# Kernel optimization log

Hardware: AMD Instinct MI355X
Metric: run time of the kernel (lower is better)

The kernel has to match this reference:

```python
import jax, jax.numpy as jnp
import numpy as np

# Levi-Civita tensor for the 1e x 1e -> 1e CG path (component normalization: eps/sqrt(2))
_e = np.zeros((3, 3, 3), dtype=np.float32)
_e[0, 1, 2] = _e[1, 2, 0] = _e[2, 0, 1] = 1.0
_e[0, 2, 1] = _e[2, 1, 0] = _e[1, 0, 2] = -1.0
EPS = jnp.asarray(_e)

B = 400000
M1S, M1V = 16, 8    # site irreps: 16x0e + 8x1e
MES, MEV = 4, 4     # edge irreps: 4x0e + 4x1e


def _split(x, mul_s, mul_v):
    # flat e3nn layout: scalars first, then vectors (xyz blocks)
    return x[:, :mul_s], x[:, mul_s:].reshape(x.shape[0], mul_v, 3)


def _fctp(x0, x1, y0, y1, W00, W11_0, W01, W10, W11_1):
    """FullyConnectedTensorProduct over irreps {0e,1e} x {0e,1e} -> {0e,1e}.
    x0:[B,u], x1:[B,u,3], y0:[B,v], y1:[B,v,3]."""
    fan0 = W00.shape[0] * W00.shape[1] + W11_0.shape[0] * W11_0.shape[1]
    out0 = (jnp.einsum('bu,bv,uvw->bw', x0, y0, W00)
            + jnp.einsum('bui,bvi,uvw->bw', x1, y1, W11_0) / np.sqrt(3.0)) / np.sqrt(fan0)
    fan1 = (W01.shape[0] * W01.shape[1] + W10.shape[0] * W10.shape[1]
            + W11_1.shape[0] * W11_1.shape[1])
    cross = jnp.einsum('bui,bvj,ijk->buvk', x1, y1, EPS)  # [B,u,v,3]
    out1 = (jnp.einsum('bu,bvi,uvw->bwi', x0, y1, W01)
            + jnp.einsum('bui,bv,uvw->bwi', x1, y0, W10)
            + jnp.einsum('buvk,uvw->bwk', cross, W11_1) / np.sqrt(2.0)) / np.sqrt(fan1)
    return out0, out1


def _forward(site1, site2, edge,
             W1_00, W1_11_0, W1_01, W1_10, W1_11_1,
             W2_00, W2_11_0, W2_01, W2_10, W2_11_1,
             W3_00, W3_11):
    x0, x1 = _split(site1, M1S, M1V)
    y0, y1 = _split(site2, M1S, M1V)
    # node-node tensor product -> 32x0e + 16x1e
    t0, t1 = _fctp(x0, x1, y0, y1, W1_00, W1_11_0, W1_01, W1_10, W1_11_1)
    e0, e1 = _split(edge, MES, MEV)
    # node-node-edge tensor product -> 64x0e + 32x1e
    u0, u1 = _fctp(t0, t1, e0, e1, W2_00, W2_11_0, W2_01, W2_10, W2_11_1)
    # Gate: 32 scalars (silu) | 32 gates (sigmoid) gating 32x1e
    s = jax.nn.silu(u0[:, :32])
    g = jax.nn.sigmoid(u0[:, 32:])
    v = u1 * g[:, :, None]
    # TensorSquare -> 1x0e (component normalization)
    fan = W3_00.shape[0] * W3_00.shape[1] + W3_11.shape[0] * W3_11.shape[1]
    out = (jnp.einsum('bu,bv,uvw->bw', s, s, W3_00)
           + jnp.einsum('bui,bvi,uvw->bw', v, v, W3_11) / np.sqrt(3.0)) / np.sqrt(fan)
    return out


def setup_inputs() -> dict:
    key = jax.random.key(0)
    ks = jax.random.split(key, 16)
    f32 = jnp.float32
    return {
        'site1': jax.random.normal(ks[0], (B, M1S + 3 * M1V), f32),
        'site2': jax.random.normal(ks[1], (B, M1S + 3 * M1V), f32),
        'edge': jax.random.normal(ks[2], (B, MES + 3 * MEV), f32),
        'W1_00': jax.random.normal(ks[3], (16, 16, 32), f32),
        'W1_11_0': jax.random.normal(ks[4], (8, 8, 32), f32),
        'W1_01': jax.random.normal(ks[5], (16, 8, 16), f32),
        'W1_10': jax.random.normal(ks[6], (8, 16, 16), f32),
        'W1_11_1': jax.random.normal(ks[7], (8, 8, 16), f32),
        'W2_00': jax.random.normal(ks[8], (32, 4, 64), f32),
        'W2_11_0': jax.random.normal(ks[9], (16, 4, 64), f32),
        'W2_01': jax.random.normal(ks[10], (32, 4, 32), f32),
        'W2_10': jax.random.normal(ks[11], (16, 4, 32), f32),
        'W2_11_1': jax.random.normal(ks[12], (16, 4, 32), f32),
        'W3_00': jax.random.normal(ks[13], (32, 32, 1), f32),
        'W3_11': jax.random.normal(ks[14], (32, 32, 1), f32),
    }


def reference(site1, site2, edge,
              W1_00, W1_11_0, W1_01, W1_10, W1_11_1,
              W2_00, W2_11_0, W2_01, W2_10, W2_11_1,
              W3_00, W3_11):
    return _forward(site1, site2, edge,
                    W1_00, W1_11_0, W1_01, W1_10, W1_11_1,
                    W2_00, W2_11_0, W2_01, W2_10, W2_11_1,
                    W3_00, W3_11)
```

## Files before the change

### kernel.cpp

```cpp
#include <hip/hip_runtime.h>


#define TPB 128

__device__ __forceinline__ float sigf(float x) {
    return 1.0f / (1.0f + __expf(-x));
}

__global__ __launch_bounds__(TPB, 2)
void intersite_fused(const float* __restrict__ site1,
                     const float* __restrict__ site2,
                     const float* __restrict__ edge,
                     const float* __restrict__ W1_00,
                     const float* __restrict__ W1_11_0,
                     const float* __restrict__ W1_01,
                     const float* __restrict__ W1_10,
                     const float* __restrict__ W1_11_1,
                     const float* __restrict__ W2_00,
                     const float* __restrict__ W2_11_0,
                     const float* __restrict__ W2_01,
                     const float* __restrict__ W2_10,
                     const float* __restrict__ W2_11_1,
                     const float* __restrict__ W3_00,
                     const float* __restrict__ W3_11,
                     float* __restrict__ out, int B)
{
    __shared__ float lds[80 * TPB];
    const int t = threadIdx.x;
    const int b = blockIdx.x * TPB + t;
    if (b >= B) return;

#define LDSF(f) lds[(f) * TPB + t]

    const float inv_s3   = 0.57735026918962576f;
    const float inv_s2   = 0.70710678118654752f;
    const float inv_s320 = 0.05590169943749474f;
    const float inv_s192 = 0.07216878364870323f;
    const float inv_s256 = 0.0625f;
    const float inv_s2048= 0.02209708691207961f;

    {
        const float4* p1 = (const float4*)(site1 + (size_t)b * 40);
        #pragma unroll
        for (int q = 0; q < 10; ++q) {
            float4 r = p1[q];
            LDSF(q*4+0) = r.x; LDSF(q*4+1) = r.y;
            LDSF(q*4+2) = r.z; LDSF(q*4+3) = r.w;
        }
        const float4* p2 = (const float4*)(site2 + (size_t)b * 40);
        #pragma unroll
        for (int q = 0; q < 10; ++q) {
            float4 r = p2[q];
            LDSF(40+q*4+0) = r.x; LDSF(40+q*4+1) = r.y;
            LDSF(40+q*4+2) = r.z; LDSF(40+q*4+3) = r.w;
        }
    }

    float t0[32];
    #pragma unroll
    for (int k = 0; k < 32; ++k) t0[k] = 0.0f;

    #pragma unroll 1
    for (int u = 0; u < 16; ++u) {
        float xu = LDSF(u);
        const float* wu = W1_00 + u * 512;
        #pragma unroll
        for (int v = 0; v < 16; ++v) {
            float f = xu * LDSF(40 + v);
            #pragma unroll
            for (int k = 0; k < 32; ++k) t0[k] = fmaf(f, wu[v*32+k], t0[k]);
        }
    }
    #pragma unroll 1
    for (int u = 0; u < 8; ++u) {
        float ax = LDSF(16+u*3), ay = LDSF(17+u*3), az = LDSF(18+u*3);
        const float* wu = W1_11_0 + u * 256;
        #pragma unroll
        for (int v = 0; v < 8; ++v) {
            float d = ax * LDSF(56+v*3);
            d = fmaf(ay, LDSF(57+v*3), d);
            d = fmaf(az, LDSF(58+v*3), d);
            d *= inv_s3;
            #pragma unroll
            for (int k = 0; k < 32; ++k) t0[k] = fmaf(d, wu[v*32+k], t0[k]);
        }
    }
    #pragma unroll
    for (int k = 0; k < 32; ++k) t0[k] *= inv_s320;

    float t1[48];
    #pragma unroll
    for (int j = 0; j < 48; ++j) t1[j] = 0.0f;

    #pragma unroll 1
    for (int u = 0; u < 16; ++u) {
        float xu = LDSF(u);
        const float* wu = W1_01 + u * 128;
        #pragma unroll
        for (int v = 0; v < 8; ++v) {
            float f0 = xu * LDSF(56+v*3+0);
            float f1 = xu * LDSF(56+v*3+1);
            float f2 = xu * LDSF(56+v*3+2);
            #pragma unroll
            for (int k = 0; k < 16; ++k) {
                float w = wu[v*16+k];
                t1[k*3+0] = fmaf(f0, w, t1[k*3+0]);
                t1[k*3+1] = fmaf(f1, w, t1[k*3+1]);
                t1[k*3+2] = fmaf(f2, w, t1[k*3+2]);
            }
        }
    }
    #pragma unroll 1
    for (int u = 0; u < 8; ++u) {
        float ax = LDSF(16+u*3), ay = LDSF(17+u*3), az = LDSF(18+u*3);
        const float* wu = W1_10 + u * 256;
        #pragma unroll
        for (int v = 0; v < 16; ++v) {
            float yv = LDSF(40 + v);
            float f0 = ax*yv, f1 = ay*yv, f2 = az*yv;
            #pragma unroll
            for (int k = 0; k < 16; ++k) {
                float w = wu[v*16+k];
                t1[k*3+0] = fmaf(f0, w, t1[k*3+0]);
                t1[k*3+1] = fmaf(f1, w, t1[k*3+1]);
                t1[k*3+2] = fmaf(f2, w, t1[k*3+2]);
            }
        }
    }
    #pragma unroll 1
    for (int u = 0; u < 8; ++u) {
        float ax = LDSF(16+u*3), ay = LDSF(17+u*3), az = LDSF(18+u*3);
        const float* wu = W1_11_1 + u * 128;
        #pragma unroll
        for (int v = 0; v < 8; ++v) {
            float bx = LDSF(56+v*3), by = LDSF(57+v*3), bz = LDSF(58+v*3);
            float cx = (ay*bz - az*by) * inv_s2;
            float cy = (az*bx - ax*bz) * inv_s2;
            float cz = (ax*by - ay*bx) * inv_s2;
            #pragma unroll
            for (int k = 0; k < 16; ++k) {
                float w = wu[v*16+k];
                t1[k*3+0] = fmaf(cx, w, t1[k*3+0]);
                t1[k*3+1] = fmaf(cy, w, t1[k*3+1]);
                t1[k*3+2] = fmaf(cz, w, t1[k*3+2]);
            }
        }
    }
    #pragma unroll
    for (int j = 0; j < 48; ++j) t1[j] *= inv_s320;

    #pragma unroll
    for (int k = 0; k < 32; ++k) LDSF(k) = t0[k];
    #pragma unroll
    for (int j = 0; j < 48; ++j) LDSF(32 + j) = t1[j];

    float e0r[4], e1r[12];
    {
        const float4* pe = (const float4*)(edge + (size_t)b * 16);
        float4 r0 = pe[0], r1 = pe[1], r2 = pe[2], r3 = pe[3];
        e0r[0]=r0.x; e0r[1]=r0.y; e0r[2]=r0.z; e0r[3]=r0.w;
        e1r[0]=r1.x; e1r[1]=r1.y; e1r[2]=r1.z; e1r[3]=r1.w;
        e1r[4]=r2.x; e1r[5]=r2.y; e1r[6]=r2.z; e1r[7]=r2.w;
        e1r[8]=r3.x; e1r[9]=r3.y; e1r[10]=r3.z; e1r[11]=r3.w;
    }

    float acc0 = 0.0f;
    {
        float ua[32];
        #pragma unroll
        for (int k = 0; k < 32; ++k) ua[k] = 0.0f;
        #pragma unroll 2
        for (int u = 0; u < 32; ++u) {
            float tu = LDSF(u);
            const float* wu = W2_00 + u*256;
            #pragma unroll
            for (int v = 0; v < 4; ++v) {
                float f = tu * e0r[v];
                #pragma unroll
                for (int k = 0; k < 32; ++k) ua[k] = fmaf(f, wu[v*64+k], ua[k]);
            }
        }
        #pragma unroll 2
        for (int u = 0; u < 16; ++u) {
            float a0 = LDSF(32+u*3), a1 = LDSF(33+u*3), a2 = LDSF(34+u*3);
            const float* wu = W2_11_0 + u*256;
            #pragma unroll
            for (int v = 0; v < 4; ++v) {
                float d = a0 * e1r[v*3];
                d = fmaf(a1, e1r[v*3+1], d);
                d = fmaf(a2, e1r[v*3+2], d);
                d *= inv_s3;
                #pragma unroll
                for (int k = 0; k < 32; ++k) ua[k] = fmaf(d, wu[v*64+k], ua[k]);
            }
        }
        #pragma unroll
        for (int k = 0; k < 32; ++k) {
            float x = ua[k] * inv_s192;
            ua[k] = x * sigf(x);
        }
        float zs[32];
        #pragma unroll
        for (int k = 0; k < 32; ++k) zs[k] = 0.0f;
        #pragma unroll
        for (int u = 0; u < 32; ++u) {
            const float* w = W3_00 + u*32;
            #pragma unroll
            for (int k = 0; k < 32; ++k) zs[k] = fmaf(ua[u], w[k], zs[k]);
        }
        #pragma unroll
        for (int k = 0; k < 32; ++k) acc0 = fmaf(zs[k], ua[k], acc0);
    }

    float g[32];
    {
        float ub[32];
        #pragma unroll
        for (int k = 0; k < 32; ++k) ub[k] = 0.0f;
        #pragma unroll 2
        for (int u = 0; u < 32; ++u) {
            float tu = LDSF(u);
            const float* wu = W2_00 + u*256 + 32;
            #pragma unroll
            for (int v = 0; v < 4; ++v) {
                float f = tu * e0r[v];
                #pragma unroll
                for (int k = 0; k < 32; ++k) ub[k] = fmaf(f, wu[v*64+k], ub[k]);
            }
        }
        #pragma unroll 2
        for (int u = 0; u < 16; ++u) {
            float a0 = LDSF(32+u*3), a1 = LDSF(33+u*3), a2 = LDSF(34+u*3);
            const float* wu = W2_11_0 + u*256 + 32;
            #pragma unroll
            for (int v = 0; v < 4; ++v) {
                float d = a0 * e1r[v*3];
                d = fmaf(a1, e1r[v*3+1], d);
                d = fmaf(a2, e1r[v*3+2], d);
                d *= inv_s3;
                #pragma unroll
                for (int k = 0; k < 32; ++k) ub[k] = fmaf(d, wu[v*64+k], ub[k]);
            }
        }
        #pragma unroll
        for (int k = 0; k < 32; ++k) g[k] = sigf(ub[k] * inv_s192);
    }

    float acc1 = 0.0f;
    const float* ep = edge + (size_t)b * 16 + 4;
    #pragma unroll 1
    for (int i = 0; i < 3; ++i) {
        int jj = (i == 2) ? 0 : i + 1;
        int kk = (jj == 2) ? 0 : jj + 1;
        float e1i[4], e1j[4], e1k[4];
        #pragma unroll
        for (int v = 0; v < 4; ++v) {
            e1i[v] = ep[v*3 + i];
            e1j[v] = ep[v*3 + jj];
            e1k[v] = ep[v*3 + kk];
        }
        float u1i[32];
        #pragma unroll
        for (int k = 0; k < 32; ++k) u1i[k] = 0.0f;

        #pragma unroll 2
        for (int u = 0; u < 32; ++u) {
            float tu = LDSF(u);
            const float* wu = W2_01 + u*128;
            #pragma unroll
            for (int v = 0; v < 4; ++v) {
                float f = tu * e1i[v];
                #pragma unroll
                for (int k = 0; k < 32; ++k) u1i[k] = fmaf(f, wu[v*32+k], u1i[k]);
            }
        }
        #pragma unroll 2
        for (int u = 0; u < 16; ++u) {
            float ai = LDSF(32 + u*3 + i);
            const float* wu = W2_10 + u*128;
            #pragma unroll
            for (int v = 0; v < 4; ++v) {
                float f = ai * e0r[v];
                #pragma unroll
                for (int k = 0; k < 32; ++k) u1i[k] = fmaf(f, wu[v*32+k], u1i[k]);
            }
        }
        #pragma unroll 2
        for (int u = 0; u < 16; ++u) {
            float aj = LDSF(32 + u*3 + jj);
            float ak = LDSF(32 + u*3 + kk);
            const float* wu = W2_11_1 + u*128;
            #pragma unroll
            for (int v = 0; v < 4; ++v) {
                float c = (aj * e1k[v] - ak * e1j[v]) * inv_s2;
                #pragma unroll
                for (int k = 0; k < 32; ++k) u1i[k] = fmaf(c, wu[v*32+k], u1i[k]);
            }
        }
        #pragma unroll
        for (int k = 0; k < 32; ++k) u1i[k] = u1i[k] * inv_s256 * g[k];
        float zv[32];
        #pragma unroll
        for (int k = 0; k < 32; ++k) zv[k] = 0.0f;
        #pragma unroll
        for (int u = 0; u < 32; ++u) {
            const float* w = W3_11 + u*32;
            #pragma unroll
            for (int k = 0; k < 32; ++k) zv[k] = fmaf(u1i[u], w[k], zv[k]);
        }
        #pragma unroll
        for (int k = 0; k < 32; ++k) acc1 = fmaf(zv[k], u1i[k], acc1);
    }

    out[b] = (acc0 + acc1 * inv_s3) * inv_s2048;
#undef LDSF
}

extern "C" void kernel_launch(void* const* d_in, const int* in_sizes, int n_in,
                              void* d_out, int out_size, void* d_ws, size_t ws_size,
                              hipStream_t stream)
{
    const float* site1   = (const float*)d_in[0];
    const float* site2   = (const float*)d_in[1];
    const float* edge    = (const float*)d_in[2];
    const float* W1_00   = (const float*)d_in[3];
    const float* W1_11_0 = (const float*)d_in[4];
    const float* W1_01   = (const float*)d_in[5];
    const float* W1_10   = (const float*)d_in[6];
    const float* W1_11_1 = (const float*)d_in[7];
    const float* W2_00   = (const float*)d_in[8];
    const float* W2_11_0 = (const float*)d_in[9];
    const float* W2_01   = (const float*)d_in[10];
    const float* W2_10   = (const float*)d_in[11];
    const float* W2_11_1 = (const float*)d_in[12];
    const float* W3_00   = (const float*)d_in[13];
    const float* W3_11   = (const float*)d_in[14];
    float* out = (float*)d_out;

    const int B = in_sizes[0] / 40;
    dim3 grid((B + TPB - 1) / TPB), block(TPB);
    hipLaunchKernelGGL(intersite_fused, grid, block, 0, stream,
                       site1, site2, edge,
                       W1_00, W1_11_0, W1_01, W1_10, W1_11_1,
                       W2_00, W2_11_0, W2_01, W2_10, W2_11_1,
                       W3_00, W3_11, out, B);
}
```

Baseline: 1.292 ms.

## Merge TP loops, precompute edge-independent W2_01 contraction, and split W3 quadratic form

Merges the first tensor product's separate u-loops so each x scalar and vector is read once per u, computing t0 and t1 together. The second stage now accumulates all 64 scalar outputs in one pass instead of two, and precomputes A2 = t0·W2_01 (128 values) once rather than recomputing it for each of the three xyz components. It also fuses the W2_10 and W2_11_1 loops and splits the W3 quadratic form into halves to reduce live registers. The cost is higher register pressure from the 64- and 128-element arrays, which risks spilling or lower occupancy.

```diff
diff --git a/kernel.cpp b/kernel.cpp
--- a/kernel.cpp
+++ b/kernel.cpp
@@ -59,22 +59,39 @@
     float t0[32];
     #pragma unroll
     for (int k = 0; k < 32; ++k) t0[k] = 0.0f;
+    float t1[48];
+    #pragma unroll
+    for (int j = 0; j < 48; ++j) t1[j] = 0.0f;
 
     #pragma unroll 1
     for (int u = 0; u < 16; ++u) {
         float xu = LDSF(u);
-        const float* wu = W1_00 + u * 512;
+        const float* w00 = W1_00 + u * 512;
         #pragma unroll
         for (int v = 0; v < 16; ++v) {
             float f = xu * LDSF(40 + v);
             #pragma unroll
-            for (int k = 0; k < 32; ++k) t0[k] = fmaf(f, wu[v*32+k], t0[k]);
+            for (int k = 0; k < 32; ++k) t0[k] = fmaf(f, w00[v*32+k], t0[k]);
+        }
+        const float* w01 = W1_01 + u * 128;
+        #pragma unroll
+        for (int v = 0; v < 8; ++v) {
+            float f0 = xu * LDSF(56+v*3+0);
+            float f1 = xu * LDSF(56+v*3+1);
+            float f2 = xu * LDSF(56+v*3+2);
+            #pragma unroll
+            for (int k = 0; k < 16; ++k) {
+                float w = w01[v*16+k];
+                t1[k*3+0] = fmaf(f0, w, t1[k*3+0]);
+                t1[k*3+1] = fmaf(f1, w, t1[k*3+1]);
+                t1[k*3+2] = fmaf(f2, w, t1[k*3+2]);
+            }
         }
     }
     #pragma unroll 1
     for (int u = 0; u < 8; ++u) {
         float ax = LDSF(16+u*3), ay = LDSF(17+u*3), az = LDSF(18+u*3);
-        const float* wu = W1_11_0 + u * 256;
+        const float* w110 = W1_11_0 + u * 256;
         #pragma unroll
         for (int v = 0; v < 8; ++v) {
             float d = ax * LDSF(56+v*3);
@@ -82,55 +99,22 @@
             d = fmaf(az, LDSF(58+v*3), d);
             d *= inv_s3;
             #pragma unroll
-            for (int k = 0; k < 32; ++k) t0[k] = fmaf(d, wu[v*32+k], t0[k]);
-        }
-    }
-    #pragma unroll
-    for (int k = 0; k < 32; ++k) t0[k] *= inv_s320;
-
-    float t1[48];
-    #pragma unroll
-    for (int j = 0; j < 48; ++j) t1[j] = 0.0f;
-
-    #pragma unroll 1
-    for (int u = 0; u < 16; ++u) {
-        float xu = LDSF(u);
-        const float* wu = W1_01 + u * 128;
-        #pragma unroll
-        for (int v = 0; v < 8; ++v) {
-            float f0 = xu * LDSF(56+v*3+0);
-            float f1 = xu * LDSF(56+v*3+1);
-            float f2 = xu * LDSF(56+v*3+2);
+            for (int k = 0; k < 32; ++k) t0[k] = fmaf(d, w110[v*32+k], t0[k]);
+        }
+        const float* w10 = W1_10 + u * 256;
+        #pragma unroll
+        for (int v = 0; v < 16; ++v) {
+            float yv = LDSF(40 + v);
+            float f0 = ax*yv, f1 = ay*yv, f2 = az*yv;
             #pragma unroll
             for (int k = 0; k < 16; ++k) {
-                float w = wu[v*16+k];
+                float w = w10[v*16+k];
                 t1[k*3+0] = fmaf(f0, w, t1[k*3+0]);
                 t1[k*3+1] = fmaf(f1, w, t1[k*3+1]);
                 t1[k*3+2] = fmaf(f2, w, t1[k*3+2]);
             }
         }
-    }
-    #pragma unroll 1
-    for (int u = 0; u < 8; ++u) {
-        float ax = LDSF(16+u*3), ay = LDSF(17+u*3), az = LDSF(18+u*3);
-        const float* wu = W1_10 + u * 256;
-        #pragma unroll
-        for (int v = 0; v < 16; ++v) {
-            float yv = LDSF(40 + v);
-            float f0 = ax*yv, f1 = ay*yv, f2 = az*yv;
-            #pragma unroll
-            for (int k = 0; k < 16; ++k) {
-                float w = wu[v*16+k];
-                t1[k*3+0] = fmaf(f0, w, t1[k*3+0]);
-                t1[k*3+1] = fmaf(f1, w, t1[k*3+1]);
-                t1[k*3+2] = fmaf(f2, w, t1[k*3+2]);
-            }
-        }
-    }
-    #pragma unroll 1
-    for (int u = 0; u < 8; ++u) {
-        float ax = LDSF(16+u*3), ay = LDSF(17+u*3), az = LDSF(18+u*3);
-        const float* wu = W1_11_1 + u * 128;
+        const float* w111 = W1_11_1 + u * 128;
         #pragma unroll
         for (int v = 0; v < 8; ++v) {
             float bx = LDSF(56+v*3), by = LDSF(57+v*3), bz = LDSF(58+v*3);
@@ -139,13 +123,15 @@
             float cz = (ax*by - ay*bx) * inv_s2;
             #pragma unroll
             for (int k = 0; k < 16; ++k) {
-                float w = wu[v*16+k];
+                float w = w111[v*16+k];
                 t1[k*3+0] = fmaf(cx, w, t1[k*3+0]);
                 t1[k*3+1] = fmaf(cy, w, t1[k*3+1]);
                 t1[k*3+2] = fmaf(cz, w, t1[k*3+2]);
             }
         }
     }
+    #pragma unroll
+    for (int k = 0; k < 32; ++k) t0[k] *= inv_s320;
     #pragma unroll
     for (int j = 0; j < 48; ++j) t1[j] *= inv_s320;
 
@@ -164,86 +150,68 @@
         e1r[8]=r3.x; e1r[9]=r3.y; e1r[10]=r3.z; e1r[11]=r3.w;
     }
 
+    float u0a[64];
+    #pragma unroll
+    for (int k = 0; k < 64; ++k) u0a[k] = 0.0f;
+    #pragma unroll 2
+    for (int u = 0; u < 32; ++u) {
+        float tu = LDSF(u);
+        const float* wu = W2_00 + u*256;
+        #pragma unroll
+        for (int v = 0; v < 4; ++v) {
+            float f = tu * e0r[v];
+            #pragma unroll
+            for (int k = 0; k < 64; ++k) u0a[k] = fmaf(f, wu[v*64+k], u0a[k]);
+        }
+    }
+    #pragma unroll 2
+    for (int u = 0; u < 16; ++u) {
+        float a0 = LDSF(32+u*3), a1 = LDSF(33+u*3), a2 = LDSF(34+u*3);
+        const float* wu = W2_11_0 + u*256;
+        #pragma unroll
+        for (int v = 0; v < 4; ++v) {
+            float d = a0 * e1r[v*3];
+            d = fmaf(a1, e1r[v*3+1], d);
+            d = fmaf(a2, e1r[v*3+2], d);
+            d *= inv_s3;
+            #pragma unroll
+            for (int k = 0; k < 64; ++k) u0a[k] = fmaf(d, wu[v*64+k], u0a[k]);
+        }
+    }
+
+    float g[32];
+    #pragma unroll
+    for (int k = 0; k < 32; ++k) g[k] = sigf(u0a[32+k] * inv_s192);
+    #pragma unroll
+    for (int k = 0; k < 32; ++k) {
+        float x = u0a[k] * inv_s192;
+        u0a[k] = x * sigf(x);
+    }
     float acc0 = 0.0f;
-    {
-        float ua[32];
-        #pragma unroll
-        for (int k = 0; k < 32; ++k) ua[k] = 0.0f;
-        #pragma unroll 2
+    #pragma unroll
+    for (int h = 0; h < 2; ++h) {
+        float zs[16];
+        #pragma unroll
+        for (int j = 0; j < 16; ++j) zs[j] = 0.0f;
+        #pragma unroll
         for (int u = 0; u < 32; ++u) {
-            float tu = LDSF(u);
-            const float* wu = W2_00 + u*256;
-            #pragma unroll
-            for (int v = 0; v < 4; ++v) {
-                float f = tu * e0r[v];
-                #pragma unroll
-                for (int k = 0; k < 32; ++k) ua[k] = fmaf(f, wu[v*64+k], ua[k]);
-            }
-        }
-        #pragma unroll 2
-        for (int u = 0; u < 16; ++u) {
-            float a0 = LDSF(32+u*3), a1 = LDSF(33+u*3), a2 = LDSF(34+u*3);
-            const float* wu = W2_11_0 + u*256;
-            #pragma unroll
-            for (int v = 0; v < 4; ++v) {
-                float d = a0 * e1r[v*3];
-                d = fmaf(a1, e1r[v*3+1], d);
-                d = fmaf(a2, e1r[v*3+2], d);
-                d *= inv_s3;
-                #pragma unroll
-                for (int k = 0; k < 32; ++k) ua[k] = fmaf(d, wu[v*64+k], ua[k]);
-            }
-        }
-        #pragma unroll
-        for (int k = 0; k < 32; ++k) {
-            float x = ua[k] * inv_s192;
-            ua[k] = x * sigf(x);
-        }
-        float zs[32];
-        #pragma unroll
-        for (int k = 0; k < 32; ++k) zs[k] = 0.0f;
-        #pragma unroll
-        for (int u = 0; u < 32; ++u) {
-            const float* w = W3_00 + u*32;
-            #pragma unroll
-            for (int k = 0; k < 32; ++k) zs[k] = fmaf(ua[u], w[k], zs[k]);
-        }
-        #pragma unroll
-        for (int k = 0; k < 32; ++k) acc0 = fmaf(zs[k], ua[k], acc0);
-    }
-
-    float g[32];
-    {
-        float ub[32];
-        #pragma unroll
-        for (int k = 0; k < 32; ++k) ub[k] = 0.0f;
-        #pragma unroll 2
-        for (int u = 0; u < 32; ++u) {
-            float tu = LDSF(u);
-            const float* wu = W2_00 + u*256 + 32;
-            #pragma unroll
-            for (int v = 0; v < 4; ++v) {
-                float f = tu * e0r[v];
-                #pragma unroll
-                for (int k = 0; k < 32; ++k) ub[k] = fmaf(f, wu[v*64+k], ub[k]);
-            }
-        }
-        #pragma unroll 2
-        for (int u = 0; u < 16; ++u) {
-            float a0 = LDSF(32+u*3), a1 = LDSF(33+u*3), a2 = LDSF(34+u*3);
-            const float* wu = W2_11_0 + u*256 + 32;
-            #pragma unroll
-            for (int v = 0; v < 4; ++v) {
-                float d = a0 * e1r[v*3];
-                d = fmaf(a1, e1r[v*3+1], d);
-                d = fmaf(a2, e1r[v*3+2], d);
-                d *= inv_s3;
-                #pragma unroll
-                for (int k = 0; k < 32; ++k) ub[k] = fmaf(d, wu[v*64+k], ub[k]);
-            }
-        }
-        #pragma unroll
-        for (int k = 0; k < 32; ++k) g[k] = sigf(ub[k] * inv_s192);
+            const float* w = W3_00 + u*32 + h*16;
+            #pragma unroll
+            for (int j = 0; j < 16; ++j) zs[j] = fmaf(u0a[u], w[j], zs[j]);
+        }
+        #pragma unroll
+        for (int j = 0; j < 16; ++j) acc0 = fmaf(zs[j], u0a[h*16+j], acc0);
+    }
+
+    float A2[128];
+    #pragma unroll
+    for (int j = 0; j < 128; ++j) A2[j] = 0.0f;
+    #pragma unroll 4
+    for (int u = 0; u < 32; ++u) {
+        float tu = LDSF(u);
+        const float* w = W2_01 + u*128;
+        #pragma unroll
+        for (int j = 0; j < 128; ++j) A2[j] = fmaf(tu, w[j], A2[j]);
     }
 
     float acc1 = 0.0f;
@@ -252,64 +220,54 @@
     for (int i = 0; i < 3; ++i) {
         int jj = (i == 2) ? 0 : i + 1;
         int kk = (jj == 2) ? 0 : jj + 1;
-        float e1i[4], e1j[4], e1k[4];
+        float e1i[4], e1j[4], e1k4[4];
         #pragma unroll
         for (int v = 0; v < 4; ++v) {
-            e1i[v] = ep[v*3 + i];
-            e1j[v] = ep[v*3 + jj];
-            e1k[v] = ep[v*3 + kk];
+            e1i[v]  = ep[v*3 + i];
+            e1j[v]  = ep[v*3 + jj];
+            e1k4[v] = ep[v*3 + kk];
         }
         float u1i[32];
         #pragma unroll
-        for (int k = 0; k < 32; ++k) u1i[k] = 0.0f;
-
-        #pragma unroll 2
-        for (int u = 0; u < 32; ++u) {
-            float tu = LDSF(u);
-            const float* wu = W2_01 + u*128;
-            #pragma unroll
-            for (int v = 0; v < 4; ++v) {
-                float f = tu * e1i[v];
-                #pragma unroll
-                for (int k = 0; k < 32; ++k) u1i[k] = fmaf(f, wu[v*32+k], u1i[k]);
-            }
-        }
+        for (int k = 0; k < 32; ++k) u1i[k] = A2[k] * e1i[0];
+        #pragma unroll
+        for (int v = 1; v < 4; ++v)
+            #pragma unroll
+            for (int k = 0; k < 32; ++k)
+                u1i[k] = fmaf(A2[v*32+k], e1i[v], u1i[k]);
+
         #pragma unroll 2
         for (int u = 0; u < 16; ++u) {
             float ai = LDSF(32 + u*3 + i);
-            const float* wu = W2_10 + u*128;
+            float aj = LDSF(32 + u*3 + jj);
+            float ak = LDSF(32 + u*3 + kk);
+            const float* wa = W2_10   + u*128;
+            const float* wb = W2_11_1 + u*128;
             #pragma unroll
             for (int v = 0; v < 4; ++v) {
                 float f = ai * e0r[v];
+                float c = (aj * e1k4[v] - ak * e1j[v]) * inv_s2;
                 #pragma unroll
-                for (int k = 0; k < 32; ++k) u1i[k] = fmaf(f, wu[v*32+k], u1i[k]);
-            }
-        }
-        #pragma unroll 2
-        for (int u = 0; u < 16; ++u) {
-            float aj = LDSF(32 + u*3 + jj);
-            float ak = LDSF(32 + u*3 + kk);
-            const float* wu = W2_11_1 + u*128;
-            #pragma unroll
-            for (int v = 0; v < 4; ++v) {
-                float c = (aj * e1k[v] - ak * e1j[v]) * inv_s2;
+                for (int k = 0; k < 32; ++k)
+                    u1i[k] = fmaf(f, wa[v*32+k], fmaf(c, wb[v*32+k], u1i[k]));
+            }
+        }
+        #pragma unroll
+        for (int k = 0; k < 32; ++k) u1i[k] = u1i[k] * inv_s256 * g[k];
+        #pragma unroll
+        for (int h = 0; h < 2; ++h) {
+            float zv[16];
+            #pragma unroll
+            for (int j = 0; j < 16; ++j) zv[j] = 0.0f;
+            #pragma unroll
+            for (int u = 0; u < 32; ++u) {
+                const float* w = W3_11 + u*32 + h*16;
                 #pragma unroll
-                for (int k = 0; k < 32; ++k) u1i[k] = fmaf(c, wu[v*32+k], u1i[k]);
-            }
-        }
-        #pragma unroll
-        for (int k = 0; k < 32; ++k) u1i[k] = u1i[k] * inv_s256 * g[k];
-        float zv[32];
-        #pragma unroll
-        for (int k = 0; k < 32; ++k) zv[k] = 0.0f;
-        #pragma unroll
-        for (int u = 0; u < 32; ++u) {
-            const float* w = W3_11 + u*32;
-            #pragma unroll
-            for (int k = 0; k < 32; ++k) zv[k] = fmaf(u1i[u], w[k], zv[k]);
-        }
-        #pragma unroll
-        for (int k = 0; k < 32; ++k) acc1 = fmaf(zv[k], u1i[k], acc1);
+                for (int j = 0; j < 16; ++j) zv[j] = fmaf(u1i[u], w[j], zv[j]);
+            }
+            #pragma unroll
+            for (int j = 0; j < 16; ++j) acc1 = fmaf(zv[j], u1i[h*16+j], acc1);
+        }
     }
 
     out[b] = (acc0 + acc1 * inv_s3) * inv_s2048;
```

Result: slower. 1.848 ms (+43.0%).

## Store per-thread LDS staging in fp16, keep site2 in registers, raise occupancy

Applied to the files above, without the earlier changes.

The per-thread LDS staging is halved by storing site1 and the intermediate t0/t1 activations as packed half2 instead of float. site2 scalars and vectors now live in registers rather than LDS. Launch bounds go from 2 to 4 blocks per SM to use the freed LDS. Stage 1 is reordered to compute t1 before t0, and the W2_10 and W2_11_1 loops are fused. The aim is higher occupancy and less LDS traffic, at the cost of fp16 rounding of intermediates (accuracy risk) and more register pressure from the added register arrays under the tighter launch bound.

```diff
diff --git a/kernel.cpp b/kernel.cpp
--- a/kernel.cpp
+++ b/kernel.cpp
@@ -1,4 +1,5 @@
 #include <hip/hip_runtime.h>
+#include <hip/hip_fp16.h>
 
 
 #define TPB 128
@@ -7,7 +8,7 @@
     return 1.0f / (1.0f + __expf(-x));
 }
 
-__global__ __launch_bounds__(TPB, 2)
+__global__ __launch_bounds__(TPB, 4)
 void intersite_fused(const float* __restrict__ site1,
                      const float* __restrict__ site2,
                      const float* __restrict__ edge,
@@ -25,12 +26,15 @@
                      const float* __restrict__ W3_11,
                      float* __restrict__ out, int B)
 {
-    __shared__ float lds[80 * TPB];
+    __shared__ float lds[44 * TPB];
     const int t = threadIdx.x;
     const int b = blockIdx.x * TPB + t;
     if (b >= B) return;
 
-#define LDSF(f) lds[(f) * TPB + t]
+    const __half* ph = (const __half*)lds;
+    __half2* ph2 = (__half2*)lds;
+#define RDH(H) __half2float(ph[(((((H) >> 1) * TPB) + t) << 1) | ((H) & 1)])
+#define WRH2(D, a, bb) ph2[(D) * TPB + t] = __floats2half2_rn((a), (bb))
 
     const float inv_s3   = 0.57735026918962576f;
     const float inv_s2   = 0.70710678118654752f;
@@ -44,17 +48,82 @@
         #pragma unroll
         for (int q = 0; q < 10; ++q) {
             float4 r = p1[q];
-            LDSF(q*4+0) = r.x; LDSF(q*4+1) = r.y;
-            LDSF(q*4+2) = r.z; LDSF(q*4+3) = r.w;
-        }
+            WRH2(q*2+0, r.x, r.y);
+            WRH2(q*2+1, r.z, r.w);
+        }
+    }
+    float y0r[16], y1r[24];
+    {
         const float4* p2 = (const float4*)(site2 + (size_t)b * 40);
         #pragma unroll
-        for (int q = 0; q < 10; ++q) {
+        for (int q = 0; q < 4; ++q) {
             float4 r = p2[q];
-            LDSF(40+q*4+0) = r.x; LDSF(40+q*4+1) = r.y;
-            LDSF(40+q*4+2) = r.z; LDSF(40+q*4+3) = r.w;
-        }
-    }
+            y0r[q*4+0]=r.x; y0r[q*4+1]=r.y; y0r[q*4+2]=r.z; y0r[q*4+3]=r.w;
+        }
+        #pragma unroll
+        for (int q = 0; q < 6; ++q) {
+            float4 r = p2[4+q];
+            y1r[q*4+0]=r.x; y1r[q*4+1]=r.y; y1r[q*4+2]=r.z; y1r[q*4+3]=r.w;
+        }
+    }
+
+    float t1[48];
+    #pragma unroll
+    for (int j = 0; j < 48; ++j) t1[j] = 0.0f;
+
+    #pragma unroll 1
+    for (int u = 0; u < 16; ++u) {
+        float xu = RDH(u);
+        const float* w01 = W1_01 + u * 128;
+        #pragma unroll
+        for (int v = 0; v < 8; ++v) {
+            float f0 = xu * y1r[v*3+0];
+            float f1 = xu * y1r[v*3+1];
+            float f2 = xu * y1r[v*3+2];
+            #pragma unroll
+            for (int k = 0; k < 16; ++k) {
+                float w = w01[v*16+k];
+                t1[k*3+0] = fmaf(f0, w, t1[k*3+0]);
+                t1[k*3+1] = fmaf(f1, w, t1[k*3+1]);
+                t1[k*3+2] = fmaf(f2, w, t1[k*3+2]);
+            }
+        }
+    }
+    #pragma unroll 1
+    for (int u = 0; u < 8; ++u) {
+        float ax = RDH(16+u*3+0), ay = RDH(16+u*3+1), az = RDH(16+u*3+2);
+        const float* w10 = W1_10 + u * 256;
+        #pragma unroll
+        for (int v = 0; v < 16; ++v) {
+            float yv = y0r[v];
+            float f0 = ax*yv, f1 = ay*yv, f2 = az*yv;
+            #pragma unroll
+            for (int k = 0; k < 16; ++k) {
+                float w = w10[v*16+k];
+                t1[k*3+0] = fmaf(f0, w, t1[k*3+0]);
+                t1[k*3+1] = fmaf(f1, w, t1[k*3+1]);
+                t1[k*3+2] = fmaf(f2, w, t1[k*3+2]);
+            }
+        }
+        const float* w111 = W1_11_1 + u * 128;
+        #pragma unroll
+        for (int v = 0; v < 8; ++v) {
+            float bx = y1r[v*3], by = y1r[v*3+1], bz = y1r[v*3+2];
+            float cx = (ay*bz - az*by) * inv_s2;
+            float cy = (az*bx - ax*bz) * inv_s2;
+            float cz = (ax*by - ay*bx) * inv_s2;
+            #pragma unroll
+            for (int k = 0; k < 16; ++k) {
+                float w = w111[v*16+k];
+                t1[k*3+0] = fmaf(cx, w, t1[k*3+0]);
+                t1[k*3+1] = fmaf(cy, w, t1[k*3+1]);
+                t1[k*3+2] = fmaf(cz, w, t1[k*3+2]);
+            }
+        }
+    }
+    #pragma unroll
+    for (int m = 0; m < 24; ++m)
+        WRH2(20 + m, t1[2*m] * inv_s320, t1[2*m+1] * inv_s320);
 
     float t0[32];
     #pragma unroll
@@ -62,97 +131,32 @@
 
     #pragma unroll 1
     for (int u = 0; u < 16; ++u) {
-        float xu = LDSF(u);
-        const float* wu = W1_00 + u * 512;
+        float xu = RDH(u);
+        const float* w00 = W1_00 + u * 512;
         #pragma unroll
         for (int v = 0; v < 16; ++v) {
-            float f = xu * LDSF(40 + v);
-            #pragma unroll
-            for (int k = 0; k < 32; ++k) t0[k] = fmaf(f, wu[v*32+k], t0[k]);
+            float f = xu * y0r[v];
+            #pragma unroll
+            for (int k = 0; k < 32; ++k) t0[k] = fmaf(f, w00[v*32+k], t0[k]);
         }
     }
     #pragma unroll 1
     for (int u = 0; u < 8; ++u) {
-        float ax = LDSF(16+u*3), ay = LDSF(17+u*3), az = LDSF(18+u*3);
-        const float* wu = W1_11_0 + u * 256;
+        float ax = RDH(16+u*3+0), ay = RDH(16+u*3+1), az = RDH(16+u*3+2);
+        const float* w110 = W1_11_0 + u * 256;
         #pragma unroll
         for (int v = 0; v < 8; ++v) {
-            float d = ax * LDSF(56+v*3);
-            d = fmaf(ay, LDSF(57+v*3), d);
-            d = fmaf(az, LDSF(58+v*3), d);
+            float d = ax * y1r[v*3];
+            d = fmaf(ay, y1r[v*3+1], d);
+            d = fmaf(az, y1r[v*3+2], d);
             d *= inv_s3;
             #pragma unroll
-            for (int k = 0; k < 32; ++k) t0[k] = fmaf(d, wu[v*32+k], t0[k]);
+            for (int k = 0; k < 32; ++k) t0[k] = fmaf(d, w110[v*32+k], t0[k]);
         }
     }
     #pragma unroll
-    for (int k = 0; k < 32; ++k) t0[k] *= inv_s320;
-
-    float t1[48];
-    #pragma unroll
-    for (int j = 0; j < 48; ++j) t1[j] = 0.0f;
-
-    #pragma unroll 1
-    for (int u = 0; u < 16; ++u) {
-        float xu = LDSF(u);
-        const float* wu = W1_01 + u * 128;
-        #pragma unroll
-        for (int v = 0; v < 8; ++v) {
-            float f0 = xu * LDSF(56+v*3+0);
-            float f1 = xu * LDSF(56+v*3+1);
-            float f2 = xu * LDSF(56+v*3+2);
-            #pragma unroll
-            for (int k = 0; k < 16; ++k) {
-                float w = wu[v*16+k];
-                t1[k*3+0] = fmaf(f0, w, t1[k*3+0]);
-                t1[k*3+1] = fmaf(f1, w, t1[k*3+1]);
-                t1[k*3+2] = fmaf(f2, w, t1[k*3+2]);
-            }
-        }
-    }
-    #pragma unroll 1
-    for (int u = 0; u < 8; ++u) {
-        float ax = LDSF(16+u*3), ay = LDSF(17+u*3), az = LDSF(18+u*3);
-        const float* wu = W1_10 + u * 256;
-        #pragma unroll
-        for (int v = 0; v < 16; ++v) {
-            float yv = LDSF(40 + v);
-            float f0 = ax*yv, f1 = ay*yv, f2 = az*yv;
-            #pragma unroll
-            for (int k = 0; k < 16; ++k) {
-                float w = wu[v*16+k];
-                t1[k*3+0] = fmaf(f0, w, t1[k*3+0]);
-                t1[k*3+1] = fmaf(f1, w, t1[k*3+1]);
-                t1[k*3+2] = fmaf(f2, w, t1[k*3+2]);
-            }
-        }
-    }
-    #pragma unroll 1
-    for (int u = 0; u < 8; ++u) {
-        float ax = LDSF(16+u*3), ay = LDSF(17+u*3), az = LDSF(18+u*3);
-        const float* wu = W1_11_1 + u * 128;
-        #pragma unroll
-        for (int v = 0; v < 8; ++v) {
-            float bx = LDSF(56+v*3), by = LDSF(57+v*3), bz = LDSF(58+v*3);
-            float cx = (ay*bz - az*by) * inv_s2;
-            float cy = (az*bx - ax*bz) * inv_s2;
-            float cz = (ax*by - ay*bx) * inv_s2;
-            #pragma unroll
-            for (int k = 0; k < 16; ++k) {
-                float w = wu[v*16+k];
-                t1[k*3+0] = fmaf(cx, w, t1[k*3+0]);
-                t1[k*3+1] = fmaf(cy, w, t1[k*3+1]);
-                t1[k*3+2] = fmaf(cz, w, t1[k*3+2]);
-            }
-        }
-    }
-    #pragma unroll
-    for (int j = 0; j < 48; ++j) t1[j] *= inv_s320;
-
-    #pragma unroll
-    for (int k = 0; k < 32; ++k) LDSF(k) = t0[k];
-    #pragma unroll
-    for (int j = 0; j < 48; ++j) LDSF(32 + j) = t1[j];
+    for (int m = 0; m < 16; ++m)
+        WRH2(m, t0[2*m] * inv_s320, t0[2*m+1] * inv_s320);
 
     float e0r[4], e1r[12];
     {
@@ -171,7 +175,7 @@
         for (int k = 0; k < 32; ++k) ua[k] = 0.0f;
         #pragma unroll 2
         for (int u = 0; u < 32; ++u) {
-            float tu = LDSF(u);
+            float tu = RDH(u);
             const float* wu = W2_00 + u*256;
             #pragma unroll
             for (int v = 0; v < 4; ++v) {
@@ -182,7 +186,7 @@
         }
         #pragma unroll 2
         for (int u = 0; u < 16; ++u) {
-            float a0 = LDSF(32+u*3), a1 = LDSF(33+u*3), a2 = LDSF(34+u*3);
+            float a0 = RDH(40+u*3+0), a1 = RDH(40+u*3+1), a2 = RDH(40+u*3+2);
             const float* wu = W2_11_0 + u*256;
             #pragma unroll
             for (int v = 0; v < 4; ++v) {
@@ -219,7 +223,7 @@
         for (int k = 0; k < 32; ++k) ub[k] = 0.0f;
         #pragma unroll 2
         for (int u = 0; u < 32; ++u) {
-            float tu = LDSF(u);
+            float tu = RDH(u);
             const float* wu = W2_00 + u*256 + 32;
             #pragma unroll
             for (int v = 0; v < 4; ++v) {
@@ -230,7 +234,7 @@
         }
         #pragma unroll 2
         for (int u = 0; u < 16; ++u) {
-            float a0 = LDSF(32+u*3), a1 = LDSF(33+u*3), a2 = LDSF(34+u*3);
+            float a0 = RDH(40+u*3+0), a1 = RDH(40+u*3+1), a2 = RDH(40+u*3+2);
             const float* wu = W2_11_0 + u*256 + 32;
             #pragma unroll
             for (int v = 0; v < 4; ++v) {
@@ -252,12 +256,12 @@
     for (int i = 0; i < 3; ++i) {
         int jj = (i == 2) ? 0 : i + 1;
         int kk = (jj == 2) ? 0 : jj + 1;
-        float e1i[4], e1j[4], e1k[4];
+        float e1i[4], e1j[4], e1k4[4];
         #pragma unroll
         for (int v = 0; v < 4; ++v) {
-            e1i[v] = ep[v*3 + i];
-            e1j[v] = ep[v*3 + jj];
-            e1k[v] = ep[v*3 + kk];
+            e1i[v]  = ep[v*3 + i];
+            e1j[v]  = ep[v*3 + jj];
+            e1k4[v] = ep[v*3 + kk];
         }
         float u1i[32];
         #pragma unroll
@@ -265,7 +269,7 @@
 
         #pragma unroll 2
         for (int u = 0; u < 32; ++u) {
-            float tu = LDSF(u);
+            float tu = RDH(u);
             const float* wu = W2_01 + u*128;
             #pragma unroll
             for (int v = 0; v < 4; ++v) {
@@ -276,25 +280,18 @@
         }
         #pragma unroll 2
         for (int u = 0; u < 16; ++u) {
-            float ai = LDSF(32 + u*3 + i);
-            const float* wu = W2_10 + u*128;
+            float ai = RDH(40 + u*3 + i);
+            float aj = RDH(40 + u*3 + jj);
+            float ak = RDH(40 + u*3 + kk);
+            const float* wa = W2_10   + u*128;
+            const float* wb = W2_11_1 + u*128;
             #pragma unroll
             for (int v = 0; v < 4; ++v) {
                 float f = ai * e0r[v];
-                #pragma unroll
-                for (int k = 0; k < 32; ++k) u1i[k] = fmaf(f, wu[v*32+k], u1i[k]);
-            }
-        }
-        #pragma unroll 2
-        for (int u = 0; u < 16; ++u) {
-            float aj = LDSF(32 + u*3 + jj);
-            float ak = LDSF(32 + u*3 + kk);
-            const float* wu = W2_11_1 + u*128;
-            #pragma unroll
-            for (int v = 0; v < 4; ++v) {
-                float c = (aj * e1k[v] - ak * e1j[v]) * inv_s2;
-                #pragma unroll
-                for (int k = 0; k < 32; ++k) u1i[k] = fmaf(c, wu[v*32+k], u1i[k]);
+                float c = (aj * e1k4[v] - ak * e1j[v]) * inv_s2;
+                #pragma unroll
+                for (int k = 0; k < 32; ++k)
+                    u1i[k] = fmaf(f, wa[v*32+k], fmaf(c, wb[v*32+k], u1i[k]));
             }
         }
         #pragma unroll
@@ -313,7 +310,8 @@
     }
 
     out[b] = (acc0 + acc1 * inv_s3) * inv_s2048;
-#undef LDSF
+#undef RDH
+#undef WRH2
 }
 
 extern "C" void kernel_launch(void* const* d_in, const int* in_sizes, int n_in,
```

After: 1.369 ms. 1.06x slower.
